# Performance work log

Hardware: AMD Instinct MI355X
Metric: run time of the kernel (lower is better)

## Reference

```python
import jax, jax.numpy as jnp
import numpy as np
from jax import lax

B, T, IN_DIM, HIDDEN = 8, 4096, 1024, 1024


def setup_inputs() -> dict:
    key = jax.random.key(0)
    k_x, k_wd, k_wb = jax.random.split(key, 3)
    x = jax.random.normal(k_x, (B, T, IN_DIM), dtype=jnp.float32)
    h0 = jnp.zeros((B, HIDDEN), dtype=jnp.float32)
    # nn.Linear default init ~ U(-1/sqrt(in), 1/sqrt(in)); b_proj.weight ~ N(0, 0.02)
    lim = 1.0 / np.sqrt(IN_DIM)
    Wd = jax.random.uniform(k_wd, (HIDDEN, IN_DIM), jnp.float32, -lim, lim)
    bd = jnp.zeros((HIDDEN,), dtype=jnp.float32)
    Wb = 0.02 * jax.random.normal(k_wb, (HIDDEN, IN_DIM), dtype=jnp.float32)
    bb = jnp.zeros((HIDDEN,), dtype=jnp.float32)
    # 'hasani' init: A_log = log(linspace(0.5, 2.0, hidden))
    A_log = jnp.log(jnp.linspace(0.5, 2.0, HIDDEN, dtype=jnp.float32))
    return {"x": x, "h0": h0, "Wd": Wd, "bd": bd, "Wb": Wb, "bb": bb, "A_log": A_log}


def _combine(c1, c2):
    # composition of affine maps h -> a*h + b
    a1, b1 = c1
    a2, b2 = c2
    return a1 * a2, a2 * b1 + b2


def reference(x, h0, Wd, bd, Wb, bb, A_log):
    # projections: (B,T,in) @ (in,hidden)
    delta = jax.nn.softplus(jnp.einsum('bti,hi->bth', x, Wd) + bd)
    b_t = delta * (jnp.einsum('bti,hi->bth', x, Wb) + bb)
    A = jnp.exp(A_log)                      # (H,) decay rate
    A_t = jnp.exp(-delta * A)               # (B,T,H)
    # parallel (Blelloch/Heinsen-style) associative scan over T:
    # cumulative affine maps give h_t = A_cum_t * h0 + B_cum_t
    A_cum, B_cum = lax.associative_scan(_combine, (A_t, b_t), axis=1)
    h_full = A_cum * h0[:, None, :] + B_cum  # (B,T,H)
    return jnp.tanh(h_full)                  # bound=True
```

## Files before the change

kernel.cpp:

```cpp
#include <hip/hip_runtime.h>
#include <math.h>

#define B_DIM 8
#define T_DIM 4096
#define K_DIM 1024
#define H_DIM 1024
#define M_DIM (B_DIM * T_DIM)
#define BK 64
#define NTT 256

#define NX8 (M_DIM * K_DIM / 8)
#define NW8 (H_DIM * K_DIM / 8)
#define NCVT (NX8 + 2 * NW8)

typedef short bf16x8 __attribute__((ext_vector_type(8)));
typedef float f32x4  __attribute__((ext_vector_type(4)));

__device__ __forceinline__ unsigned short f2bf(float f) {
  unsigned int u = __builtin_bit_cast(unsigned int, f);
  u += 0x7FFFu + ((u >> 16) & 1u);
  return (unsigned short)(u >> 16);
}

__device__ __forceinline__ void gload_lds16(const void* g, void* l) {
  __builtin_amdgcn_global_load_lds(
      (const __attribute__((address_space(1))) unsigned int*)g,
      (__attribute__((address_space(3))) unsigned int*)l, 16, 0, 0);
}

__device__ __forceinline__ float softplus_fast(float x) {
  float e = __expf(-fabsf(x));
  return fmaxf(x, 0.f) + __logf(1.f + e);
}

__device__ __forceinline__ float tanh_fast(float x) {
  float e = __expf(2.f * x);
  return 1.f - 2.f * __builtin_amdgcn_rcpf(e + 1.f);
}

__global__ __launch_bounds__(256) void k_cvt3(const float* __restrict__ x,
                                              const float* __restrict__ Wd,
                                              const float* __restrict__ Wb,
                                              unsigned short* __restrict__ xb,
                                              unsigned short* __restrict__ wdb,
                                              unsigned short* __restrict__ wbb) {
  int i = blockIdx.x * 256 + threadIdx.x;
  if (i >= NCVT) return;
  const float* src;
  unsigned short* dst;
  int j;
  if (i < NX8)                 { src = x;  dst = xb;  j = i; }
  else if (i < NX8 + NW8)      { src = Wd; dst = wdb; j = i - NX8; }
  else                         { src = Wb; dst = wbb; j = i - NX8 - NW8; }
  float4 v0 = ((const float4*)src)[j * 2 + 0];
  float4 v1 = ((const float4*)src)[j * 2 + 1];
  bf16x8 r;
  r[0] = (short)f2bf(v0.x); r[1] = (short)f2bf(v0.y);
  r[2] = (short)f2bf(v0.z); r[3] = (short)f2bf(v0.w);
  r[4] = (short)f2bf(v1.x); r[5] = (short)f2bf(v1.y);
  r[6] = (short)f2bf(v1.z); r[7] = (short)f2bf(v1.w);
  ((bf16x8*)dst)[j] = r;
}

__global__ __launch_bounds__(256, 2) void k_mega(
    const unsigned short* __restrict__ Xb,
    const unsigned short* __restrict__ Wdb,
    const unsigned short* __restrict__ Wbb,
    const float* __restrict__ bd,
    const float* __restrict__ bb,
    const float* __restrict__ A_log,
    const float* __restrict__ h0,
    float* __restrict__ out)
{
  __shared__ unsigned short As[2][256 * BK];
  __shared__ unsigned short Bs[2][32 * BK];
  __shared__ float totA[4][16], totB[4][16];
  __shared__ float h_state[16];

  const int tid   = threadIdx.x;
  const int wg    = blockIdx.x;
  const int batch = wg & 7;
  const int jn    = wg >> 3;
  const int bn    = jn * 16;

  const int w    = tid >> 6;
  const int lane = tid & 63;
  const int c    = w;
  const int fr   = lane & 15;
  const int hi   = lane >> 4;
  const int gcol = bn + fr;

  const float bdv = bd[gcol];
  const float bbv = bb[gcol];
  const float Ah  = __expf(A_log[gcol]);

  const unsigned short* gA[8];
  int ldsA[8];
#pragma unroll
  for (int jj = 0; jj < 8; jj++) {
    int idx = jj * 256 + tid;
    int row = idx >> 3;
    int cg  = (idx & 7) ^ (row & 7);
    ldsA[jj] = idx * 16;
    gA[jj] = Xb + (((size_t)(batch * T_DIM + row)) << 10) + (size_t)(cg * 8);
  }
  const unsigned short* gB;
  int ldsB;
  {
    int idx = tid;
    int vr  = idx >> 3;
    int cg  = (idx & 7) ^ (vr & 7);
    ldsB = idx * 16;
    int h = bn + (vr & 15);
    const unsigned short* Wsrc = (vr & 16) ? Wbb : Wdb;
    gB = Wsrc + (((size_t)h) << 10) + (size_t)(cg * 8);
  }

  const int ch0 = hi ^ (fr & 7);
  const char* bA0 = (const char*)As + ((c * 64 + fr) * 128 + ch0 * 16);
  const char* bA1 = (const char*)As + ((c * 64 + fr) * 128 + (ch0 ^ 4) * 16);
  const char* bB0 = (const char*)Bs + (fr * 128 + ch0 * 16);
  const char* bB1 = (const char*)Bs + (fr * 128 + (ch0 ^ 4) * 16);

#define STAGE(TT, D)                                                          \
  do {                                                                        \
    int aOff = (((TT) >> 4) << 18) + (((TT) & 15) << 6);                      \
    int bOff = ((TT) & 15) << 6;                                              \
    _Pragma("unroll")                                                         \
    for (int jj = 0; jj < 8; jj++)                                            \
      gload_lds16(gA[jj] + aOff, (char*)As[D] + ldsA[jj]);                    \
    gload_lds16(gB + bOff, (char*)Bs[D] + ldsB);                              \
  } while (0)

#define TILE(TT, D)                                                           \
  do {                                                                        \
    if ((TT) < NTT - 1) STAGE((TT) + 1, (D) ^ 1);                             \
    bf16x8 Af[8], Bf[4];                                                      \
    _Pragma("unroll")                                                         \
    for (int mm = 0; mm < 4; mm++) {                                          \
      Af[mm * 2 + 0] = *(const bf16x8*)(bA0 + (D) * 32768 + mm * 2048);       \
      Af[mm * 2 + 1] = *(const bf16x8*)(bA1 + (D) * 32768 + mm * 2048);       \
    }                                                                         \
    _Pragma("unroll")                                                         \
    for (int nn = 0; nn < 2; nn++) {                                          \
      Bf[nn * 2 + 0] = *(const bf16x8*)(bB0 + (D) * 4096 + nn * 2048);        \
      Bf[nn * 2 + 1] = *(const bf16x8*)(bB1 + (D) * 4096 + nn * 2048);        \
    }                                                                         \
    __builtin_amdgcn_s_setprio(1);                                            \
    _Pragma("unroll")                                                         \
    for (int mm = 0; mm < 4; mm++)                                            \
      _Pragma("unroll")                                                       \
      for (int nn = 0; nn < 2; nn++)                                          \
        _Pragma("unroll")                                                     \
        for (int kk = 0; kk < 2; kk++)                                        \
          acc[mm][nn] = __builtin_amdgcn_mfma_f32_16x16x32_bf16(              \
              Af[mm * 2 + kk], Bf[nn * 2 + kk], acc[mm][nn], 0, 0, 0);        \
    __builtin_amdgcn_s_setprio(0);                                            \
    asm volatile("s_waitcnt vmcnt(0)" ::: "memory");                          \
    __builtin_amdgcn_s_barrier();                                             \
  } while (0)

  STAGE(0, 0);
  if (tid < 16) h_state[tid] = h0[(batch << 10) + bn + tid];
  asm volatile("s_waitcnt vmcnt(0)" ::: "memory");
  __syncthreads();

  const f32x4 z4 = {0.f, 0.f, 0.f, 0.f};

#pragma unroll 1
  for (int mt = 0; mt < 16; mt++) {
    f32x4 acc[4][2];
#pragma unroll
    for (int m = 0; m < 4; m++) { acc[m][0] = z4; acc[m][1] = z4; }

#pragma unroll 1
    for (int kp = 0; kp < 8; kp++) {
      int tt = mt * 16 + kp * 2;
      TILE(tt, 0);
      TILE(tt + 1, 1);
    }

    float rA[4], rB[4], wAp[4][4], wBp[4][4];
#pragma unroll
    for (int m = 0; m < 4; m++) {
      float A_ = 1.f, B_ = 0.f;
#pragma unroll
      for (int r = 0; r < 4; r++) {
        float z1  = acc[m][0][r] + bdv;
        float z2  = acc[m][1][r] + bbv;
        float dlt = softplus_fast(z1);
        float av  = __expf(-dlt * Ah);
        float bv  = dlt * z2;
        B_ = fmaf(av, B_, bv);
        A_ *= av;
        wAp[m][r] = A_; wBp[m][r] = B_;
      }
      rA[m] = A_; rB[m] = B_;
    }
    float cA = 1.f, cB = 0.f, eA[4], eB[4];
#pragma unroll
    for (int rho = 0; rho < 16; rho++) {
      if ((rho & 3) == hi) { eA[rho >> 2] = cA; eB[rho >> 2] = cB; }
      float sa = __shfl(rA[rho >> 2], (rho & 3) * 16 + fr, 64);
      float sb = __shfl(rB[rho >> 2], (rho & 3) * 16 + fr, 64);
      cB = fmaf(sa, cB, sb);
      cA *= sa;
    }
    if (hi == 0) { totA[c][fr] = cA; totB[c][fr] = cB; }
    __syncthreads();
    float hs = h_state[fr];
#pragma unroll
    for (int cc = 0; cc < 3; cc++) {
      float t2 = fmaf(totA[cc][fr], hs, totB[cc][fr]);
      hs = (cc < c) ? t2 : hs;
    }
    __syncthreads();
    if (c == 3 && hi == 0) h_state[fr] = fmaf(cA, hs, cB);

    size_t obase = (((size_t)(batch * T_DIM + mt * 256 + c * 64 + hi * 4)) << 10)
                   + (size_t)gcol;
#pragma unroll
    for (int m = 0; m < 4; m++) {
#pragma unroll
      for (int r = 0; r < 4; r++) {
        float aT = eA[m] * wAp[m][r];
        float bT = fmaf(wAp[m][r], eB[m], wBp[m][r]);
        float h  = fmaf(aT, hs, bT);
        out[obase + ((size_t)(m * 16 + r) << 10)] = tanh_fast(h);
      }
    }
  }
#undef TILE
#undef STAGE
}

extern "C" void kernel_launch(void* const* d_in, const int* in_sizes, int n_in,
                              void* d_out, int out_size, void* d_ws, size_t ws_size,
                              hipStream_t stream) {
  const float* x     = (const float*)d_in[0];
  const float* h0    = (const float*)d_in[1];
  const float* Wd    = (const float*)d_in[2];
  const float* bd    = (const float*)d_in[3];
  const float* Wb    = (const float*)d_in[4];
  const float* bb    = (const float*)d_in[5];
  const float* A_log = (const float*)d_in[6];
  float* out = (float*)d_out;

  char* ws = (char*)d_ws;
  unsigned short* xb  = (unsigned short*)(ws + 0);
  unsigned short* wdb = (unsigned short*)(ws + 67108864);
  unsigned short* wbb = (unsigned short*)(ws + 69206016);

  k_cvt3<<<(NCVT + 255) / 256, 256, 0, stream>>>(x, Wd, Wb, xb, wdb, wbb);

  k_mega<<<512, 256, 0, stream>>>(xb, wdb, wbb, bd, bb, A_log, h0, out);
}
```

Before: 299.3 us.

## Prefetch next M-tile's K-slices during scan epilogue and use lighter barriers

Restructures the K-loop so the first two K-slices of the next 256-row tile are issued before the scan/tanh epilogue runs, hiding the global-to-LDS load latency behind epilogue math and stores. The inner loop is fully unrolled with a peeled first and last compute step. The __syncthreads in the epilogue are replaced with raw s_barrier plus lgkmcnt waits, so pending global loads are not drained at those points. The trade-off is a larger code footprint and an extra vmcnt wait and barrier at the end of each tile, which also waits on the output stores.

```diff
diff --git a/kernel.cpp b/kernel.cpp
--- a/kernel.cpp
+++ b/kernel.cpp
@@ -7,7 +7,6 @@
 #define H_DIM 1024
 #define M_DIM (B_DIM * T_DIM)
 #define BK 64
-#define NTT 256
 
 #define NX8 (M_DIM * K_DIM / 8)
 #define NW8 (H_DIM * K_DIM / 8)
@@ -37,6 +36,13 @@
   float e = __expf(2.f * x);
   return 1.f - 2.f * __builtin_amdgcn_rcpf(e + 1.f);
 }
+
+#define RAW_BAR()                                                             \
+  do {                                                                        \
+    asm volatile("s_waitcnt lgkmcnt(0)" ::: "memory");                        \
+    __builtin_amdgcn_sched_barrier(0);                                        \
+    __builtin_amdgcn_s_barrier();                                             \
+  } while (0)
 
 __global__ __launch_bounds__(256) void k_cvt3(const float* __restrict__ x,
                                               const float* __restrict__ Wd,
@@ -132,9 +138,8 @@
     gload_lds16(gB + bOff, (char*)Bs[D] + ldsB);                              \
   } while (0)
 
-#define TILE(TT, D)                                                           \
-  do {                                                                        \
-    if ((TT) < NTT - 1) STAGE((TT) + 1, (D) ^ 1);                             \
+#define COMPUTE(D)                                                            \
+  do {                                                                        \
     bf16x8 Af[8], Bf[4];                                                      \
     _Pragma("unroll")                                                         \
     for (int mm = 0; mm < 4; mm++) {                                          \
@@ -156,11 +161,18 @@
           acc[mm][nn] = __builtin_amdgcn_mfma_f32_16x16x32_bf16(              \
               Af[mm * 2 + kk], Bf[nn * 2 + kk], acc[mm][nn], 0, 0, 0);        \
     __builtin_amdgcn_s_setprio(0);                                            \
+  } while (0)
+
+#define TILE_N(TT, D)                                                         \
+  do {                                                                        \
+    STAGE((TT) + 1, (D) ^ 1);                                                 \
+    COMPUTE(D);                                                               \
     asm volatile("s_waitcnt vmcnt(0)" ::: "memory");                          \
     __builtin_amdgcn_s_barrier();                                             \
   } while (0)
 
   STAGE(0, 0);
+  STAGE(1, 1);
   if (tid < 16) h_state[tid] = h0[(batch << 10) + bn + tid];
   asm volatile("s_waitcnt vmcnt(0)" ::: "memory");
   __syncthreads();
@@ -169,16 +181,24 @@
 
 #pragma unroll 1
   for (int mt = 0; mt < 16; mt++) {
+    const int base = mt * 16;
     f32x4 acc[4][2];
 #pragma unroll
     for (int m = 0; m < 4; m++) { acc[m][0] = z4; acc[m][1] = z4; }
 
-#pragma unroll 1
-    for (int kp = 0; kp < 8; kp++) {
-      int tt = mt * 16 + kp * 2;
-      TILE(tt, 0);
-      TILE(tt + 1, 1);
-    }
+    COMPUTE(0);
+    __builtin_amdgcn_s_barrier();
+
+#pragma unroll
+    for (int kp = 0; kp < 7; kp++) {
+      TILE_N(base + 1 + 2 * kp, 1);
+      TILE_N(base + 2 + 2 * kp, 0);
+    }
+
+    if (mt < 15) STAGE(base + 16, 0);
+    COMPUTE(1);
+    __builtin_amdgcn_s_barrier();
+    if (mt < 15) STAGE(base + 17, 1);
 
     float rA[4], rB[4], wAp[4][4], wBp[4][4];
 #pragma unroll
@@ -207,14 +227,14 @@
       cA *= sa;
     }
     if (hi == 0) { totA[c][fr] = cA; totB[c][fr] = cB; }
-    __syncthreads();
+    RAW_BAR();
     float hs = h_state[fr];
 #pragma unroll
     for (int cc = 0; cc < 3; cc++) {
       float t2 = fmaf(totA[cc][fr], hs, totB[cc][fr]);
       hs = (cc < c) ? t2 : hs;
     }
-    __syncthreads();
+    RAW_BAR();
     if (c == 3 && hi == 0) h_state[fr] = fmaf(cA, hs, cB);
 
     size_t obase = (((size_t)(batch * T_DIM + mt * 256 + c * 64 + hi * 4)) << 10)
@@ -229,8 +249,12 @@
         out[obase + ((size_t)(m * 16 + r) << 10)] = tanh_fast(h);
       }
     }
+
+    asm volatile("s_waitcnt vmcnt(0)" ::: "memory");
+    __builtin_amdgcn_s_barrier();
   }
-#undef TILE
+#undef TILE_N
+#undef COMPUTE
 #undef STAGE
 }
 
```

Result: no change. 302.3 us (+1.0%).
